# Performance work log

Hardware: AMD Instinct MI355X
Metric: run time of the kernel (lower is better)

Reference implementation:

```python
import jax, jax.numpy as jnp
import numpy as np

NEG_INF = jnp.float32(-1e30)


def setup_inputs() -> dict:
    key = jax.random.key(0)
    k1, k2, k3, k4 = jax.random.split(key, 4)
    B, L1, L2, H = 64, 1024, 1024, 128
    x = jax.random.normal(k1, (B, L1, H), dtype=jnp.float32)
    y = jax.random.normal(k2, (B, L2, H), dtype=jnp.float32)
    y_mask = jax.random.uniform(k3, (B, L2)) < 0.2
    W = jax.random.normal(k4, (H, H), dtype=jnp.float32) * (1.0 / np.sqrt(H))
    b = jnp.zeros((H,), dtype=jnp.float32)
    return {"x": x, "y": y, "y_mask": y_mask, "W": W, "b": b}


def reference(x, y, y_mask, W, b):
    # shared linear + relu projections (torch Linear: x @ W.T + b)
    x_proj = jax.nn.relu(jnp.einsum("bld,hd->blh", x, W) + b)  # [B, L1, H]
    y_proj = jax.nn.relu(jnp.einsum("bld,hd->blh", y, W) + b)  # [B, L2, H]
    # unscaled cross-attention scores
    scores = jnp.einsum("bih,bjh->bij", x_proj, y_proj)  # [B, L1, L2]
    scores = jnp.where(y_mask[:, None, :], NEG_INF, scores)
    alpha = jax.nn.softmax(scores, axis=-1)  # [B, L1, L2]
    # weighted sum over original (unprojected) y
    matched_seq = jnp.einsum("bij,bjh->bih", alpha, y)  # [B, L1, H]
    return matched_seq
```

## Files before the change

### kernel.cpp

```cpp
#include <hip/hip_runtime.h>
#include <hip/hip_bf16.h>


typedef __attribute__((ext_vector_type(8))) short    s8v;
typedef __attribute__((ext_vector_type(8))) _Float16 h8v;
typedef __attribute__((ext_vector_type(4))) _Float16 h4v;
typedef __attribute__((ext_vector_type(4))) float    f4v;

#define BDIM 256

__device__ __forceinline__ f4v mfma_bf16(s8v a, s8v b, f4v c) {
    return __builtin_amdgcn_mfma_f32_16x16x32_bf16(a, b, c, 0, 0, 0);
}
__device__ __forceinline__ f4v mfma_f16(h8v a, h8v b, f4v c) {
    return __builtin_amdgcn_mfma_f32_16x16x32_f16(a, b, c, 0, 0, 0);
}
__device__ __forceinline__ void tsplit(float v, short& hi, short& lo) {
    unsigned b = __builtin_bit_cast(unsigned, v);
    unsigned hb = b & 0xFFFF0000u;
    float res = v - __builtin_bit_cast(float, hb);
    hi = (short)(hb >> 16);
    lo = (short)(__builtin_bit_cast(unsigned, res) >> 16);
}

typedef const __attribute__((address_space(1))) unsigned int gu32;
typedef __attribute__((address_space(3))) unsigned int lu32;
__device__ __forceinline__ void gld_lds16(const void* g, void* l) {
    __builtin_amdgcn_global_load_lds((gu32*)g, (lu32*)l, 16, 0, 0);
}

__global__ __launch_bounds__(1024) void prep_kernel(
    const unsigned int* __restrict__ mraw, unsigned char* __restrict__ nm,
    const float* __restrict__ W, short* __restrict__ Whsw, short* __restrict__ Wlsw,
    const float* __restrict__ Y, _Float16* __restrict__ YTsw)
{
    if (blockIdx.x >= 2) {
        const int tb = blockIdx.x - 2;
        const int b = tb >> 4, jt = tb & 15;
        __shared__ _Float16 sT[128][64];
        const int tid = threadIdx.x;
        const int h = tid & 127, c0 = tid >> 7;
        const float* yb = Y + (size_t)(b * 1024 + jt * 64 + c0 * 8) * 128 + h;
        h8v hv;
        for (int k = 0; k < 8; ++k) hv[k] = (_Float16)yb[k * 128];
        *(h8v*)&sT[h][(c0 ^ (h & 7)) << 3] = hv;
        __syncthreads();
        *(h8v*)(YTsw + (size_t)tb * 8192 + tid * 8) =
            *(const h8v*)(&sT[0][0] + tid * 8);
        return;
    }
    if (blockIdx.x == 1) {
        for (int idx = threadIdx.x; idx < 16384; idx += 1024) {
            int r = idx >> 7, c = idx & 127;
            short hi, lo; tsplit(W[idx], hi, lo);
            int cs = (((c >> 3) ^ (r & 15)) << 3) | (c & 7);
            Whsw[r * 128 + cs] = hi;
            Wlsw[r * 128 + cs] = lo;
        }
        return;
    }
    __shared__ unsigned int sOrAll, sOrOdd;
    if (threadIdx.x == 0) { sOrAll = 0u; sOrOdd = 0u; }
    __syncthreads();
    unsigned int oa = 0u, oo = 0u;
    for (int i = threadIdx.x; i < 16384; i += 1024) {
        unsigned int v = mraw[i];
        oa |= v;
        if (i & 1) oo |= v;
    }
    atomicOr(&sOrAll, oa);
    atomicOr(&sOrOdd, oo);
    __syncthreads();
    const unsigned int orv = sOrAll, oro = sOrOdd;
    int mode;
    if (orv <= 1u)                       mode = (orv == 1u && oro == 0u) ? 3 : 0;
    else if ((orv & 0xFEFEFEFEu) == 0u)  mode = 1;
    else if ((orv & 0x0000FFFFu) == 0u)  mode = 0;
    else                                 mode = 2;
    const unsigned char*  b8  = (const unsigned char*)mraw;
    const unsigned short* b16 = (const unsigned short*)mraw;
    for (int j = threadIdx.x; j < 65536; j += 1024) {
        unsigned int v;
        if (mode == 0)      v = mraw[j];
        else if (mode == 1) v = b8[j];
        else if (mode == 2) v = b16[j];
        else                v = mraw[2 * j] | mraw[2 * j + 1];
        nm[j] = v ? 1 : 0;
    }
}

__global__ __launch_bounds__(BDIM, 4) void proj_kernel(
    const float* __restrict__ X, const float* __restrict__ Y,
    const short* __restrict__ Whsw, const short* __restrict__ Wlsw,
    const float* __restrict__ bias,
    _Float16* __restrict__ XPf, _Float16* __restrict__ YPsw)
{
    __shared__ short sW[2][64][128];

    const int gid = blockIdx.x;
    const float* src; int local;
    if (gid < 1024) { src = X; local = gid; }
    else            { src = Y; local = gid - 1024; }
    const int row0 = (local >> 1) * 128, h0 = (local & 1) * 64;
    const int t = threadIdx.x, w = t >> 6, lane = t & 63, c = lane & 15, q = lane >> 4;

    {
        const short* g0 = Whsw + h0 * 128;
        const short* g1 = Wlsw + h0 * 128;
        short* l0 = &sW[0][0][0];
        short* l1 = &sW[1][0][0];
        for (int i = 0; i < 4; ++i) {
            int off = (t + i * BDIM) * 8;
            *(s8v*)(l0 + off) = *(const s8v*)(g0 + off);
            *(s8v*)(l1 + off) = *(const s8v*)(g1 + off);
        }
    }

    f4v rawA[2][4], rawB[2][4];
#pragma unroll
    for (int set = 0; set < 2; ++set) {
        const float* xr = src + (size_t)(row0 + w * 32 + set * 16 + c) * 128;
#pragma unroll
        for (int ks = 0; ks < 4; ++ks) {
            rawA[set][ks] = *(const f4v*)&xr[ks * 32 + q * 8];
            rawB[set][ks] = *(const f4v*)&xr[ks * 32 + q * 8 + 4];
        }
    }
    __syncthreads();

    f4v zero = {0.f, 0.f, 0.f, 0.f};
#pragma unroll
    for (int set = 0; set < 2; ++set) {
        s8v ah[4], al[4];
#pragma unroll
        for (int ks = 0; ks < 4; ++ks) {
            for (int k = 0; k < 4; ++k) {
                short hh, ll;
                tsplit(rawA[set][ks][k], hh, ll); ah[ks][k] = hh;     al[ks][k] = ll;
                tsplit(rawB[set][ks][k], hh, ll); ah[ks][4 + k] = hh; al[ks][4 + k] = ll;
            }
        }
        f4v acc[4];
        for (int n = 0; n < 4; ++n) acc[n] = zero;
#pragma unroll
        for (int ks = 0; ks < 4; ++ks) {
            s8v bh[4], bl[4];
            for (int nt = 0; nt < 4; ++nt) {
                int cs = (((ks * 4 + q) ^ c) << 3);
                bh[nt] = *(const s8v*)&sW[0][nt * 16 + c][cs];
                bl[nt] = *(const s8v*)&sW[1][nt * 16 + c][cs];
            }
            for (int nt = 0; nt < 4; ++nt) {
                acc[nt] = mfma_bf16(ah[ks], bh[nt], acc[nt]);
                acc[nt] = mfma_bf16(al[ks], bh[nt], acc[nt]);
                acc[nt] = mfma_bf16(ah[ks], bl[nt], acc[nt]);
            }
        }
        for (int nt = 0; nt < 4; ++nt) {
            float bv = bias[h0 + nt * 16 + c];
            for (int r = 0; r < 4; ++r) {
                float v = fmaxf(acc[nt][r] + bv, 0.0f);
                int grow = row0 + w * 32 + set * 16 + q * 4 + r;
                int h = h0 + nt * 16 + c;
                if (gid < 1024) {
                    XPf[(size_t)grow * 128 + h] = (_Float16)v;
                } else {
                    int jt = (grow >> 6) & 15, jr = grow & 63;
                    int chunk = (h >> 3) ^ (jr & 7);
                    size_t off = (size_t)((grow >> 10) * 16 + jt) * 8192
                                 + jr * 128 + chunk * 8 + (h & 7);
                    YPsw[off] = (_Float16)v;
                }
            }
        }
    }
}

__global__ __launch_bounds__(512, 4) void attn_kernel(
    const _Float16* __restrict__ YPsw, const _Float16* __restrict__ YTsw,
    const unsigned char* __restrict__ nmask,
    const _Float16* __restrict__ XPf, float* __restrict__ out)
{
    __shared__ _Float16 sTile[2][16384];
    __shared__ _Float16 sP[128 * 64];

    const int id = blockIdx.x;
    const int xcd = id & 7, rest = id >> 3;
    const int ibase = (rest & 7) * 128;
    const int b = xcd + 8 * (rest >> 3);
    const int t = threadIdx.x, wave = t >> 6, lane = t & 63;
    const int c = lane & 15, q = lane >> 4;
    const int mrow = b * 1024;

    h8v afrag[4];
    {
        const _Float16* xr = XPf + (size_t)(mrow + ibase + wave * 16 + c) * 128;
        for (int ks = 0; ks < 4; ++ks)
            afrag[ks] = *(const h8v*)&xr[ks * 32 + q * 8];
    }

    const char* gYP = (const char*)(YPsw + (size_t)b * 16 * 8192);
    const char* gYT = (const char*)(YTsw + (size_t)b * 16 * 8192);
    const int soff = wave * 1024 + lane * 16;

    {
        char* lp = (char*)&sTile[0][0]    + wave * 1024;
        char* lt = (char*)&sTile[0][8192] + wave * 1024;
        for (int i = 0; i < 2; ++i) {
            gld_lds16(gYP + soff + i * 8192, lp + i * 8192);
            gld_lds16(gYT + soff + i * 8192, lt + i * 8192);
        }
    }

    unsigned mw[4];
    for (int nt = 0; nt < 4; ++nt)
        mw[nt] = *(const unsigned*)(nmask + mrow + nt * 16 + q * 4);

    f4v zero = {0.f, 0.f, 0.f, 0.f};
    float m_s = -INFINITY, l_s = 0.f;
    f4v o[8];
    for (int h = 0; h < 8; ++h) o[h] = zero;

    const int srcbase = (lane & 48) + ((lane >> 4) << 2);
    const int cb = q ^ (c & 7);
    const int prow = (wave * 16 + c) * 64;
    const int pwofs = (q & 1) * 4;

    __syncthreads();

    int cur = 0;
    for (int jt = 0; jt < 16; ++jt) {
        const int jbase = jt * 64;
        const int nx = cur ^ 1;

        if (jt < 15) {
            const char* gp = gYP + (size_t)(jt + 1) * 16384;
            const char* gt = gYT + (size_t)(jt + 1) * 16384;
            char* lp = (char*)&sTile[nx][0]    + wave * 1024;
            char* lt = (char*)&sTile[nx][8192] + wave * 1024;
            for (int i = 0; i < 2; ++i) {
                gld_lds16(gp + soff + i * 8192, lp + i * 8192);
                gld_lds16(gt + soff + i * 8192, lt + i * 8192);
            }
        }

        f4v s[4];
        __builtin_amdgcn_s_setprio(1);
        for (int nt = 0; nt < 4; ++nt) {
            const _Float16* rp = &sTile[cur][0] + (nt * 16 + c) * 128;
            h8v f0 = *(const h8v*)(rp + ((cb ^ 0) << 3));
            h8v f1 = *(const h8v*)(rp + ((cb ^ 4) << 3));
            h8v f2 = *(const h8v*)(rp + ((cb ^ 8) << 3));
            h8v f3 = *(const h8v*)(rp + ((cb ^ 12) << 3));
            f4v acc = zero;
            acc = mfma_f16(f0, afrag[0], acc);
            acc = mfma_f16(f1, afrag[1], acc);
            acc = mfma_f16(f2, afrag[2], acc);
            acc = mfma_f16(f3, afrag[3], acc);
            s[nt] = acc;
        }
        __builtin_amdgcn_s_setprio(0);

        for (int nt = 0; nt < 4; ++nt)
            for (int r = 0; r < 4; ++r)
                if ((mw[nt] >> (r * 8)) & 0xFFu) s[nt][r] = -1e30f;

        float mx = fmaxf(
            fmaxf(fmaxf(fmaxf(s[0][0], s[0][1]), fmaxf(s[0][2], s[0][3])),
                  fmaxf(fmaxf(s[1][0], s[1][1]), fmaxf(s[1][2], s[1][3]))),
            fmaxf(fmaxf(fmaxf(s[2][0], s[2][1]), fmaxf(s[2][2], s[2][3])),
                  fmaxf(fmaxf(s[3][0], s[3][1]), fmaxf(s[3][2], s[3][3]))));
        mx = fmaxf(mx, __shfl_xor(mx, 16, 64));
        mx = fmaxf(mx, __shfl_xor(mx, 32, 64));
        float mnew = fmaxf(m_s, mx);
        float alpha = __expf(m_s - mnew);
        m_s = mnew;

        float rsum = 0.f;
        for (int nt = 0; nt < 4; ++nt) {
            h4v ph4;
            for (int r = 0; r < 4; ++r) {
                float p = ((mw[nt] >> (r * 8)) & 0xFFu) ? 0.f
                          : __expf(s[nt][r] - mnew);
                _Float16 ph = (_Float16)p;
                rsum += (float)ph;
                ph4[r] = ph;
            }
            int ck = (2 * nt + (q >> 1)) ^ (c & 7);
            *(h4v*)&sP[prow + ck * 8 + pwofs] = ph4;
        }
        rsum += __shfl_xor(rsum, 16, 64);
        rsum += __shfl_xor(rsum, 32, 64);
        l_s = l_s * alpha + rsum;

        if (jt < 15) {
            const int jn = jbase + 64;
            for (int nt = 0; nt < 4; ++nt)
                mw[nt] = *(const unsigned*)(nmask + mrow + jn + nt * 16 + q * 4);
        }

        float aD0 = __shfl(alpha, srcbase + 0, 64);
        float aD1 = __shfl(alpha, srcbase + 1, 64);
        float aD2 = __shfl(alpha, srcbase + 2, 64);
        float aD3 = __shfl(alpha, srcbase + 3, 64);
        for (int h = 0; h < 8; ++h) {
            o[h][0] *= aD0; o[h][1] *= aD1; o[h][2] *= aD2; o[h][3] *= aD3;
        }

        __builtin_amdgcn_s_setprio(1);
        for (int k2 = 0; k2 < 2; ++k2) {
            h8v a = *(const h8v*)&sP[prow + (((k2 << 2) + q) ^ (c & 7)) * 8];
            const _Float16* yt = &sTile[cur][8192];
            for (int hb = 0; hb < 8; ++hb) {
                h8v bb = *(const h8v*)(yt + (hb * 16 + c) * 64
                                       + ((((k2 << 2) + q) ^ (c & 7)) << 3));
                o[hb] = mfma_f16(a, bb, o[hb]);
            }
        }
        __builtin_amdgcn_s_setprio(0);

        __syncthreads();
        cur = nx;
    }

    float lD[4];
    lD[0] = __shfl(l_s, srcbase + 0, 64);
    lD[1] = __shfl(l_s, srcbase + 1, 64);
    lD[2] = __shfl(l_s, srcbase + 2, 64);
    lD[3] = __shfl(l_s, srcbase + 3, 64);
    for (int h = 0; h < 8; ++h) {
        for (int r = 0; r < 4; ++r) {
            float v = o[h][r] / lD[r];
            out[(size_t)(mrow + ibase + wave * 16 + q * 4 + r) * 128 + h * 16 + c] = v;
        }
    }
}

extern "C" void kernel_launch(void* const* d_in, const int* in_sizes, int n_in,
                              void* d_out, int out_size, void* d_ws, size_t ws_size,
                              hipStream_t stream) {
    const float* x    = (const float*)d_in[0];
    const float* y    = (const float*)d_in[1];
    const unsigned int* mraw = (const unsigned int*)d_in[2];
    const float* W    = (const float*)d_in[3];
    const float* bias = (const float*)d_in[4];
    float* out = (float*)d_out;

    unsigned char* nmask = (unsigned char*)d_ws;
    short* Whsw = (short*)((char*)d_ws + 65536);
    short* Wlsw = Whsw + 16384;
    _Float16* XPf = (_Float16*)(Wlsw + 16384);
    _Float16* YPsw = XPf + (size_t)64 * 1024 * 128;
    _Float16* YTsw = YPsw + (size_t)64 * 1024 * 128;

    prep_kernel<<<1026, 1024, 0, stream>>>(mraw, nmask, W, Whsw, Wlsw, y, YTsw);
    proj_kernel<<<2048, BDIM, 0, stream>>>(x, y, Whsw, Wlsw, bias, XPf, YPsw);
    attn_kernel<<<512, 512, 0, stream>>>(YPsw, YTsw, nmask, XPf, out);
}
```

Baseline: 215.0 us.

## Fuse prep and projection kernels into one launch with in-block weight splitting

```diff
diff --git a/kernel.cpp b/kernel.cpp
--- a/kernel.cpp
+++ b/kernel.cpp
@@ -29,91 +29,88 @@
     __builtin_amdgcn_global_load_lds((gu32*)g, (lu32*)l, 16, 0, 0);
 }
 
-__global__ __launch_bounds__(1024) void prep_kernel(
-    const unsigned int* __restrict__ mraw, unsigned char* __restrict__ nm,
-    const float* __restrict__ W, short* __restrict__ Whsw, short* __restrict__ Wlsw,
-    const float* __restrict__ Y, _Float16* __restrict__ YTsw)
+__global__ __launch_bounds__(BDIM, 4) void fused_pp(
+    const float* __restrict__ X, const float* __restrict__ Y,
+    const unsigned int* __restrict__ mraw,
+    const float* __restrict__ W, const float* __restrict__ bias,
+    unsigned char* __restrict__ nm,
+    _Float16* __restrict__ XPf, _Float16* __restrict__ YPsw,
+    _Float16* __restrict__ YTsw)
 {
-    if (blockIdx.x >= 2) {
-        const int tb = blockIdx.x - 2;
+    __shared__ __attribute__((aligned(16))) char smem[32768];
+    const int gid = blockIdx.x;
+    const int t = threadIdx.x;
+
+    if (gid == 0) {
+        unsigned* sOr = (unsigned*)smem;
+        if (t == 0) { sOr[0] = 0u; sOr[1] = 0u; }
+        __syncthreads();
+        unsigned oa = 0u, oo = 0u;
+        for (int i = t; i < 16384; i += BDIM) {
+            unsigned v = mraw[i];
+            oa |= v;
+            if (i & 1) oo |= v;
+        }
+        atomicOr(&sOr[0], oa);
+        atomicOr(&sOr[1], oo);
+        __syncthreads();
+        const unsigned orv = sOr[0], oro = sOr[1];
+        int mode;
+        if (orv <= 1u)                       mode = (orv == 1u && oro == 0u) ? 3 : 0;
+        else if ((orv & 0xFEFEFEFEu) == 0u)  mode = 1;
+        else if ((orv & 0x0000FFFFu) == 0u)  mode = 0;
+        else                                 mode = 2;
+        const unsigned char*  b8  = (const unsigned char*)mraw;
+        const unsigned short* b16 = (const unsigned short*)mraw;
+        for (int j = t; j < 65536; j += BDIM) {
+            unsigned v;
+            if (mode == 0)      v = mraw[j];
+            else if (mode == 1) v = b8[j];
+            else if (mode == 2) v = b16[j];
+            else                v = mraw[2 * j] | mraw[2 * j + 1];
+            nm[j] = v ? 1 : 0;
+        }
+        return;
+    }
+
+    if (gid <= 1024) {
+        const int tb = gid - 1;
         const int b = tb >> 4, jt = tb & 15;
-        __shared__ _Float16 sT[128][64];
-        const int tid = threadIdx.x;
-        const int h = tid & 127, c0 = tid >> 7;
-        const float* yb = Y + (size_t)(b * 1024 + jt * 64 + c0 * 8) * 128 + h;
-        h8v hv;
-        for (int k = 0; k < 8; ++k) hv[k] = (_Float16)yb[k * 128];
-        *(h8v*)&sT[h][(c0 ^ (h & 7)) << 3] = hv;
+        _Float16* sT = (_Float16*)smem;
+        for (int i = 0; i < 4; ++i) {
+            int idx = t + i * BDIM;
+            int h = idx & 127, c0 = idx >> 7;
+            const float* yb = Y + (size_t)(b * 1024 + jt * 64 + c0 * 8) * 128 + h;
+            h8v hv;
+            for (int k = 0; k < 8; ++k) hv[k] = (_Float16)yb[k * 128];
+            *(h8v*)&sT[h * 64 + ((c0 ^ (h & 7)) << 3)] = hv;
+        }
         __syncthreads();
-        *(h8v*)(YTsw + (size_t)tb * 8192 + tid * 8) =
-            *(const h8v*)(&sT[0][0] + tid * 8);
+        for (int i = 0; i < 4; ++i) {
+            int idx = t + i * BDIM;
+            *(h8v*)(YTsw + (size_t)tb * 8192 + idx * 8) =
+                *(const h8v*)(sT + idx * 8);
+        }
         return;
     }
-    if (blockIdx.x == 1) {
-        for (int idx = threadIdx.x; idx < 16384; idx += 1024) {
-            int r = idx >> 7, c = idx & 127;
-            short hi, lo; tsplit(W[idx], hi, lo);
-            int cs = (((c >> 3) ^ (r & 15)) << 3) | (c & 7);
-            Whsw[r * 128 + cs] = hi;
-            Wlsw[r * 128 + cs] = lo;
-        }
-        return;
-    }
-    __shared__ unsigned int sOrAll, sOrOdd;
-    if (threadIdx.x == 0) { sOrAll = 0u; sOrOdd = 0u; }
-    __syncthreads();
-    unsigned int oa = 0u, oo = 0u;
-    for (int i = threadIdx.x; i < 16384; i += 1024) {
-        unsigned int v = mraw[i];
-        oa |= v;
-        if (i & 1) oo |= v;
-    }
-    atomicOr(&sOrAll, oa);
-    atomicOr(&sOrOdd, oo);
-    __syncthreads();
-    const unsigned int orv = sOrAll, oro = sOrOdd;
-    int mode;
-    if (orv <= 1u)                       mode = (orv == 1u && oro == 0u) ? 3 : 0;
-    else if ((orv & 0xFEFEFEFEu) == 0u)  mode = 1;
-    else if ((orv & 0x0000FFFFu) == 0u)  mode = 0;
-    else                                 mode = 2;
-    const unsigned char*  b8  = (const unsigned char*)mraw;
-    const unsigned short* b16 = (const unsigned short*)mraw;
-    for (int j = threadIdx.x; j < 65536; j += 1024) {
-        unsigned int v;
-        if (mode == 0)      v = mraw[j];
-        else if (mode == 1) v = b8[j];
-        else if (mode == 2) v = b16[j];
-        else                v = mraw[2 * j] | mraw[2 * j + 1];
-        nm[j] = v ? 1 : 0;
-    }
-}
-
-__global__ __launch_bounds__(BDIM, 4) void proj_kernel(
-    const float* __restrict__ X, const float* __restrict__ Y,
-    const short* __restrict__ Whsw, const short* __restrict__ Wlsw,
-    const float* __restrict__ bias,
-    _Float16* __restrict__ XPf, _Float16* __restrict__ YPsw)
-{
-    __shared__ short sW[2][64][128];
-
-    const int gid = blockIdx.x;
+
+    const int pl = gid - 1025;
     const float* src; int local;
-    if (gid < 1024) { src = X; local = gid; }
-    else            { src = Y; local = gid - 1024; }
+    if (pl < 1024) { src = X; local = pl; }
+    else           { src = Y; local = pl - 1024; }
     const int row0 = (local >> 1) * 128, h0 = (local & 1) * 64;
-    const int t = threadIdx.x, w = t >> 6, lane = t & 63, c = lane & 15, q = lane >> 4;
-
-    {
-        const short* g0 = Whsw + h0 * 128;
-        const short* g1 = Wlsw + h0 * 128;
-        short* l0 = &sW[0][0][0];
-        short* l1 = &sW[1][0][0];
-        for (int i = 0; i < 4; ++i) {
-            int off = (t + i * BDIM) * 8;
-            *(s8v*)(l0 + off) = *(const s8v*)(g0 + off);
-            *(s8v*)(l1 + off) = *(const s8v*)(g1 + off);
-        }
+    const int w = t >> 6, lane = t & 63, c = lane & 15, q = lane >> 4;
+
+    short* sW0 = (short*)smem;
+    short* sW1 = sW0 + 8192;
+
+    for (int i = 0; i < 32; ++i) {
+        int idx = t + i * BDIM;
+        int rr = idx >> 7, c2 = idx & 127;
+        short hi, lo; tsplit(W[(h0 + rr) * 128 + c2], hi, lo);
+        int cs = (((c2 >> 3) ^ (rr & 15)) << 3) | (c2 & 7);
+        sW0[rr * 128 + cs] = hi;
+        sW1[rr * 128 + cs] = lo;
     }
 
     f4v rawA[2][4], rawB[2][4];
@@ -147,8 +144,8 @@
             s8v bh[4], bl[4];
             for (int nt = 0; nt < 4; ++nt) {
                 int cs = (((ks * 4 + q) ^ c) << 3);
-                bh[nt] = *(const s8v*)&sW[0][nt * 16 + c][cs];
-                bl[nt] = *(const s8v*)&sW[1][nt * 16 + c][cs];
+                bh[nt] = *(const s8v*)&sW0[(nt * 16 + c) * 128 + cs];
+                bl[nt] = *(const s8v*)&sW1[(nt * 16 + c) * 128 + cs];
             }
             for (int nt = 0; nt < 4; ++nt) {
                 acc[nt] = mfma_bf16(ah[ks], bh[nt], acc[nt]);
@@ -162,7 +159,7 @@
                 float v = fmaxf(acc[nt][r] + bv, 0.0f);
                 int grow = row0 + w * 32 + set * 16 + q * 4 + r;
                 int h = h0 + nt * 16 + c;
-                if (gid < 1024) {
+                if (pl < 1024) {
                     XPf[(size_t)grow * 128 + h] = (_Float16)v;
                 } else {
                     int jt = (grow >> 6) & 15, jr = grow & 63;
@@ -347,13 +344,10 @@
     float* out = (float*)d_out;
 
     unsigned char* nmask = (unsigned char*)d_ws;
-    short* Whsw = (short*)((char*)d_ws + 65536);
-    short* Wlsw = Whsw + 16384;
-    _Float16* XPf = (_Float16*)(Wlsw + 16384);
+    _Float16* XPf = (_Float16*)((char*)d_ws + 65536);
     _Float16* YPsw = XPf + (size_t)64 * 1024 * 128;
     _Float16* YTsw = YPsw + (size_t)64 * 1024 * 128;
 
-    prep_kernel<<<1026, 1024, 0, stream>>>(mraw, nmask, W, Whsw, Wlsw, y, YTsw);
-    proj_kernel<<<2048, BDIM, 0, stream>>>(x, y, Whsw, Wlsw, bias, XPf, YPsw);
+    fused_pp<<<3073, BDIM, 0, stream>>>(x, y, mraw, W, bias, nmask, XPf, YPsw, YTsw);
     attn_kernel<<<512, 512, 0, stream>>>(YPsw, YTsw, nmask, XPf, out);
 }
```

Measured after the change: 288.4 us. +34.1%, slower.
